# Performance work log

Hardware: AMD Instinct MI355X
Metric: run time of the kernel (lower is better)

## Reference

```python
import jax, jax.numpy as jnp
import numpy as np

NEG_INF = -1e6

def setup_inputs() -> dict:
    key = jax.random.key(0)
    ks = jax.random.split(key, 7)
    B, Q, K, D, H = 16, 64, 1024, 256, 128
    return {
        "queries": jax.random.normal(ks[0], (B, Q, D), dtype=jnp.float32),
        "keys": jax.random.normal(ks[1], (B, K, D), dtype=jnp.float32),
        "values": jax.random.normal(ks[2], (B, K, D), dtype=jnp.float32),
        "valid_lens": jax.random.randint(ks[3], (B,), 1, K + 1, dtype=jnp.int32),
        "W_q": jax.random.normal(ks[4], (D, H), dtype=jnp.float32) * (1.0 / np.sqrt(D)),
        "W_k": jax.random.normal(ks[5], (D, H), dtype=jnp.float32) * (1.0 / np.sqrt(D)),
        "w_v": jax.random.normal(ks[6], (H,), dtype=jnp.float32) * (1.0 / np.sqrt(H)),
    }

def reference(queries, keys, values, valid_lens, W_q, W_k, w_v):
    # project: [B,Q,H], [B,K,H]
    q = jnp.einsum('bqd,dh->bqh', queries, W_q)
    k = jnp.einsum('bkd,dh->bkh', keys, W_k)
    # broadcast add -> tanh -> score: [B,Q,K]
    features = jnp.tanh(q[:, :, None, :] + k[:, None, :, :])  # [B,Q,K,H]
    scores = jnp.einsum('bqkh,h->bqk', features, w_v)
    # masked softmax over key axis (valid_lens per batch)
    K_len = keys.shape[1]
    mask = jnp.arange(K_len)[None, None, :] < valid_lens[:, None, None]  # [B,1,K]
    scores = jnp.where(mask, scores, NEG_INF)
    attn = jax.nn.softmax(scores, axis=-1)
    # weighted sum of values: [B,Q,Dv]  (dropout p=0 -> identity)
    return jnp.einsum('bqk,bkd->bqd', attn, values)
```

## Files before the change

kernel.cpp:

```cpp
#include <hip/hip_runtime.h>

#define DDIM 256
#define HDIM 128
#define KLEN 1024
#define SCL 2.8853900817779268f

__global__ __launch_bounds__(256) void proj_kernel(
    const float* __restrict__ queries, const float* __restrict__ keys,
    const float* __restrict__ W_q, const float* __restrict__ W_k,
    float* __restrict__ Eq, float* __restrict__ Ek)
{
    __shared__ union {
        float a[64 * 64];
        float t[32][68];
    } sm;

    const int tid  = threadIdx.x;
    const int lane = tid & 63;
    const int wav  = tid >> 6;

    int blk = blockIdx.x;
    bool iskey; int b = 0, kc0 = 0, hb, row0;
    const float* in; const float* W;
    if (blk < 1024) {
        iskey = true;
        int xcd = blk & 7, s = blk >> 3;
        b = ((s >> 6) << 3) | xcd;
        int r6 = s & 63;
        kc0 = (r6 >> 2) << 6;
        hb  = (r6 & 3) << 5;
        row0 = b * KLEN + kc0;
        in = keys; W = W_k;
    } else {
        iskey = false;
        int qrb = blk - 1024;
        row0 = (qrb >> 2) << 6;
        hb   = (qrb & 3) << 5;
        in = queries; W = W_q;
    }

    const int hg8 = __builtin_amdgcn_readfirstlane(wav << 3);
    const float* Wu = W + hb + hg8;

    const int srow = tid >> 4;
    const int sgd  = tid & 15;
    const float* gsrc = in + (size_t)(row0 + srow) * DDIM + (sgd << 2);

    float4 pf0 = *(const float4*)(gsrc);
    float4 pf1 = *(const float4*)(gsrc + 16 * DDIM);
    float4 pf2 = *(const float4*)(gsrc + 32 * DDIM);
    float4 pf3 = *(const float4*)(gsrc + 48 * DDIM);

    float acc[8];
    #pragma unroll
    for (int c = 0; c < 8; c++) acc[c] = 0.f;

    const int w0 = (srow)      * 64 + ((sgd ^ ((srow)      & 7)) << 2);
    const int w1 = (srow + 16) * 64 + ((sgd ^ ((srow + 16) & 7)) << 2);
    const int w2 = (srow + 32) * 64 + ((sgd ^ ((srow + 32) & 7)) << 2);
    const int w3 = (srow + 48) * 64 + ((sgd ^ ((srow + 48) & 7)) << 2);

    for (int dt0 = 0; dt0 < DDIM; dt0 += 64) {
        *(float4*)(sm.a + w0) = pf0;
        *(float4*)(sm.a + w1) = pf1;
        *(float4*)(sm.a + w2) = pf2;
        *(float4*)(sm.a + w3) = pf3;
        __syncthreads();
        if (dt0 < DDIM - 64) {
            const float* g2 = gsrc + dt0 + 64;
            pf0 = *(const float4*)(g2);
            pf1 = *(const float4*)(g2 + 16 * DDIM);
            pf2 = *(const float4*)(g2 + 32 * DDIM);
            pf3 = *(const float4*)(g2 + 48 * DDIM);
        }
        const float* arow = sm.a + lane * 64;
        const int lx = lane & 7;
        #pragma unroll
        for (int d4 = 0; d4 < 64; d4 += 4) {
            float4 a = *(const float4*)(arow + ((((d4 >> 2)) ^ lx) << 2));
            const float* wr = Wu + (size_t)(dt0 + d4) * HDIM;
            #pragma unroll
            for (int c = 0; c < 8; c++) acc[c] = fmaf(a.x, wr[c],            acc[c]);
            #pragma unroll
            for (int c = 0; c < 8; c++) acc[c] = fmaf(a.y, wr[HDIM + c],     acc[c]);
            #pragma unroll
            for (int c = 0; c < 8; c++) acc[c] = fmaf(a.z, wr[2 * HDIM + c], acc[c]);
            #pragma unroll
            for (int c = 0; c < 8; c++) acc[c] = fmaf(a.w, wr[3 * HDIM + c], acc[c]);
        }
        __syncthreads();
    }

    float e[8];
    #pragma unroll
    for (int c = 0; c < 8; c++) e[c] = __builtin_amdgcn_exp2f(SCL * acc[c]);

    if (!iskey) {
        float* dst = Eq + (size_t)(row0 + lane) * HDIM + hb + hg8;
        *(float4*)(dst)     = make_float4(e[0], e[1], e[2], e[3]);
        *(float4*)(dst + 4) = make_float4(e[4], e[5], e[6], e[7]);
    } else {
        #pragma unroll
        for (int c = 0; c < 8; c++) sm.t[(wav << 3) + c][lane] = e[c];
        __syncthreads();
        float* dstb = Ek + (size_t)b * HDIM * KLEN + (size_t)hb * KLEN + kc0;
        #pragma unroll
        for (int i = 0; i < 2; i++) {
            int g = tid + (i << 8);
            int h = g >> 4, k4 = (g & 15) << 2;
            float4 o = *(const float4*)(&sm.t[h][k4]);
            *(float4*)(dstb + (size_t)h * KLEN + k4) = o;
        }
    }
}

__global__ __launch_bounds__(512) void score_kernel(
    const float* __restrict__ Eq, const float* __restrict__ Ek,
    const float* __restrict__ w_v, const int* __restrict__ valid_lens,
    float* __restrict__ p)
{
    __shared__ float4 eqw[HDIM];
    __shared__ float red0[8], red1[8];

    int tid = threadIdx.x, lane = tid & 63, wav = tid >> 6;
    int blk = blockIdx.x;
    int xcd = blk & 7, s = blk >> 3;
    int b = ((s >= 32) ? 8 : 0) + xcd;
    int qp = s & 31;
    int bq0 = b * 64 + qp * 2;
    int vlen = valid_lens[b];

    if (tid < HDIM) {
        float w2 = -2.0f * w_v[tid];
        eqw[tid] = make_float4(Eq[(size_t)bq0 * HDIM + tid],
                               Eq[(size_t)(bq0 + 1) * HDIM + tid], w2, 0.f);
    }
    __syncthreads();

    int k0 = tid << 1;
    float s00 = -1e30f, s01 = -1e30f, s10 = -1e30f, s11 = -1e30f;
    if (k0 < vlen) {
        const float* ekp = Ek + (size_t)b * HDIM * KLEN + k0;
        float a00 = 0.f, a01 = 0.f, a10 = 0.f, a11 = 0.f;
        #pragma unroll 4
        for (int h = 0; h < HDIM; h++) {
            float2 ek = *(const float2*)(ekp + (size_t)h * KLEN);
            float4 e  = eqw[h];
            a00 = fmaf(e.z, __builtin_amdgcn_rcpf(fmaf(e.x, ek.x, 1.f)), a00);
            a01 = fmaf(e.z, __builtin_amdgcn_rcpf(fmaf(e.x, ek.y, 1.f)), a01);
            a10 = fmaf(e.z, __builtin_amdgcn_rcpf(fmaf(e.y, ek.x, 1.f)), a10);
            a11 = fmaf(e.z, __builtin_amdgcn_rcpf(fmaf(e.y, ek.y, 1.f)), a11);
        }
        s00 = a00; s10 = a10;
        if (k0 + 1 < vlen) { s01 = a01; s11 = a11; }
    }

    float m0 = fmaxf(s00, s01), m1 = fmaxf(s10, s11);
    #pragma unroll
    for (int off = 32; off > 0; off >>= 1) {
        m0 = fmaxf(m0, __shfl_xor(m0, off, 64));
        m1 = fmaxf(m1, __shfl_xor(m1, off, 64));
    }
    if (lane == 0) { red0[wav] = m0; red1[wav] = m1; }
    __syncthreads();
    m0 = red0[0]; m1 = red1[0];
    #pragma unroll
    for (int i = 1; i < 8; i++) {
        m0 = fmaxf(m0, red0[i]);
        m1 = fmaxf(m1, red1[i]);
    }

    float e00 = __expf(s00 - m0), e01 = __expf(s01 - m0);
    float e10 = __expf(s10 - m1), e11 = __expf(s11 - m1);
    float t0 = e00 + e01, t1 = e10 + e11;
    #pragma unroll
    for (int off = 32; off > 0; off >>= 1) {
        t0 += __shfl_xor(t0, off, 64);
        t1 += __shfl_xor(t1, off, 64);
    }
    __syncthreads();
    if (lane == 0) { red0[wav] = t0; red1[wav] = t1; }
    __syncthreads();
    t0 = red0[0]; t1 = red1[0];
    #pragma unroll
    for (int i = 1; i < 8; i++) { t0 += red0[i]; t1 += red1[i]; }
    float inv0 = 1.0f / t0, inv1 = 1.0f / t1;

    float* p0 = p + (size_t)bq0 * KLEN + k0;
    *(float2*)(p0)        = make_float2(e00 * inv0, e01 * inv0);
    *(float2*)(p0 + KLEN) = make_float2(e10 * inv1, e11 * inv1);
}

__global__ __launch_bounds__(256) void av_kernel(
    const float* __restrict__ p, const float* __restrict__ values,
    const int* __restrict__ valid_lens, float* __restrict__ part)
{
    __shared__ union {
        float  pt[512][8];
        float4 slab[4][8][64];
    } sm;

    int blk = blockIdx.x;
    int xcd = blk & 7, s = blk >> 3;
    int b = ((s >> 4) << 3) | xcd;
    int r = s & 15, qt = r >> 1, kh = r & 1;
    int tid = threadIdx.x, lane = tid & 63, w = tid >> 6;
    int vlen = valid_lens[b];
    int bq0 = b * 64 + qt * 8;
    int kbase = kh << 9;

    #pragma unroll
    for (int i = 0; i < 4; i++) {
        int slot = tid + (i << 8);
        int q = slot >> 7, k4 = (slot & 127) << 2;
        float4 pv = *(const float4*)(p + (size_t)(bq0 + q) * KLEN + kbase + k4);
        sm.pt[k4 + 0][q] = pv.x;
        sm.pt[k4 + 1][q] = pv.y;
        sm.pt[k4 + 2][q] = pv.z;
        sm.pt[k4 + 3][q] = pv.w;
    }
    __syncthreads();

    int kw = w << 7;
    int cnt = vlen - (kbase + kw); cnt = cnt < 0 ? 0 : (cnt > 128 ? 128 : cnt);
    int cnt4 = (cnt + 3) & ~3;
    const float* vb = values + ((size_t)b * KLEN + kbase + kw) * DDIM + (lane << 2);

    float4 acc[8];
    #pragma unroll
    for (int q = 0; q < 8; q++) acc[q] = make_float4(0.f, 0.f, 0.f, 0.f);

    for (int k = 0; k < cnt4; k += 4) {
        #pragma unroll
        for (int j = 0; j < 4; j++) {
            float4 v  = *(const float4*)(vb + (size_t)(k + j) * DDIM);
            float4 p0 = *(const float4*)(&sm.pt[kw + k + j][0]);
            float4 p1 = *(const float4*)(&sm.pt[kw + k + j][4]);
            float pq[8] = {p0.x, p0.y, p0.z, p0.w, p1.x, p1.y, p1.z, p1.w};
            #pragma unroll
            for (int q = 0; q < 8; q++) {
                acc[q].x = fmaf(pq[q], v.x, acc[q].x);
                acc[q].y = fmaf(pq[q], v.y, acc[q].y);
                acc[q].z = fmaf(pq[q], v.z, acc[q].z);
                acc[q].w = fmaf(pq[q], v.w, acc[q].w);
            }
        }
    }

    __syncthreads();
    #pragma unroll
    for (int q = 0; q < 8; q++) sm.slab[w][q][lane] = acc[q];
    __syncthreads();
    #pragma unroll
    for (int e = 0; e < 2; e++) {
        int slot = (tid << 1) | e;
        int q = slot >> 6, d4 = slot & 63;
        float4 a = sm.slab[0][q][d4];
        #pragma unroll
        for (int g = 1; g < 4; g++) {
            float4 t = sm.slab[g][q][d4];
            a.x += t.x; a.y += t.y; a.z += t.z; a.w += t.w;
        }
        *(float4*)(part + ((size_t)kh * 1024 + bq0 + q) * DDIM + (d4 << 2)) = a;
    }
}

__global__ __launch_bounds__(256) void combine_kernel(
    const float* __restrict__ part, float* __restrict__ out)
{
    int i = blockIdx.x * 256 + threadIdx.x;
    const float4* p4 = (const float4*)part;
    float4 a = p4[i];
    float4 v = p4[65536 + i];
    a.x += v.x; a.y += v.y; a.z += v.z; a.w += v.w;
    ((float4*)out)[i] = a;
}

extern "C" void kernel_launch(void* const* d_in, const int* in_sizes, int n_in,
                              void* d_out, int out_size, void* d_ws, size_t ws_size,
                              hipStream_t stream) {
    const float* queries    = (const float*)d_in[0];
    const float* keys       = (const float*)d_in[1];
    const float* values     = (const float*)d_in[2];
    const int*   valid_lens = (const int*)d_in[3];
    const float* W_q        = (const float*)d_in[4];
    const float* W_k        = (const float*)d_in[5];
    const float* w_v        = (const float*)d_in[6];

    float* Eq   = (float*)d_ws;
    float* Ek   = Eq + 131072;
    float* p    = Ek + 2097152;
    float* part = Ek;

    proj_kernel<<<1088, 256, 0, stream>>>(queries, keys, W_q, W_k, Eq, Ek);
    score_kernel<<<512, 512, 0, stream>>>(Eq, Ek, w_v, valid_lens, p);
    av_kernel<<<256, 256, 0, stream>>>(p, values, valid_lens, part);
    combine_kernel<<<256, 256, 0, stream>>>(part, (float*)d_out);
}
```

Measured before the change: 147.1 us.

## Tile score kernel over 4 queries with LDS-staged Ek and defer softmax normalization

```diff
diff --git a/kernel.cpp b/kernel.cpp
--- a/kernel.cpp
+++ b/kernel.cpp
@@ -114,85 +114,108 @@
     }
 }
 
-__global__ __launch_bounds__(512) void score_kernel(
+__global__ __launch_bounds__(256) void score_kernel(
     const float* __restrict__ Eq, const float* __restrict__ Ek,
     const float* __restrict__ w_v, const int* __restrict__ valid_lens,
-    float* __restrict__ p)
+    float* __restrict__ E, float* __restrict__ T)
 {
-    __shared__ float4 eqw[HDIM];
-    __shared__ float red0[8], red1[8];
-
-    int tid = threadIdx.x, lane = tid & 63, wav = tid >> 6;
-    int blk = blockIdx.x;
-    int xcd = blk & 7, s = blk >> 3;
-    int b = ((s >= 32) ? 8 : 0) + xcd;
-    int qp = s & 31;
-    int bq0 = b * 64 + qp * 2;
+    __shared__ float ekt[8][KLEN];
+    __shared__ float eqs[4][HDIM];
+    __shared__ float w2s[HDIM];
+    __shared__ float tred[4][4];
+
+    const int tid = threadIdx.x;
+    const int lane = tid & 63, wav = tid >> 6;
+    int m = blockIdx.x;
+    int xcd = m & 7, bh = (m >> 3) & 1, qg = m >> 4;
+    int b = (bh << 3) | xcd;
+    int bq0 = b * 64 + qg * 4;
+
+    if (tid < HDIM) w2s[tid] = -2.0f * w_v[tid];
+    #pragma unroll
+    for (int i = 0; i < 2; i++) {
+        int idx = tid + (i << 8);
+        int q = idx >> 7, h = idx & 127;
+        eqs[q][h] = Eq[(size_t)(bq0 + q) * HDIM + h];
+    }
+
+    const float* ekb = Ek + (size_t)b * HDIM * KLEN;
+    const int k0 = tid << 2;
+
+    float4 pf[8];
+    #pragma unroll
+    for (int i = 0; i < 8; i++)
+        pf[i] = *(const float4*)(ekb + (size_t)i * KLEN + k0);
+
+    float4 acc4[4];
+    #pragma unroll
+    for (int j = 0; j < 4; j++) acc4[j] = make_float4(0.f, 0.f, 0.f, 0.f);
+
+    for (int c = 0; c < 16; c++) {
+        __syncthreads();
+        #pragma unroll
+        for (int i = 0; i < 8; i++)
+            *(float4*)(&ekt[i][k0]) = pf[i];
+        __syncthreads();
+        if (c < 15) {
+            const float* nx = ekb + (size_t)(c + 1) * 8 * KLEN + k0;
+            #pragma unroll
+            for (int i = 0; i < 8; i++)
+                pf[i] = *(const float4*)(nx + (size_t)i * KLEN);
+        }
+        const int c8 = c << 3;
+        float eqr[4][8], w2r[8];
+        #pragma unroll
+        for (int j = 0; j < 4; j++) {
+            *(float4*)(&eqr[j][0]) = *(const float4*)(&eqs[j][c8]);
+            *(float4*)(&eqr[j][4]) = *(const float4*)(&eqs[j][c8 + 4]);
+        }
+        *(float4*)(&w2r[0]) = *(const float4*)(&w2s[c8]);
+        *(float4*)(&w2r[4]) = *(const float4*)(&w2s[c8 + 4]);
+
+        #pragma unroll
+        for (int hh = 0; hh < 8; hh++) {
+            float4 ek = *(const float4*)(&ekt[hh][k0]);
+            float w2v = w2r[hh];
+            #pragma unroll
+            for (int j = 0; j < 4; j++) {
+                float eqv = eqr[j][hh];
+                acc4[j].x = fmaf(w2v, __builtin_amdgcn_rcpf(fmaf(eqv, ek.x, 1.f)), acc4[j].x);
+                acc4[j].y = fmaf(w2v, __builtin_amdgcn_rcpf(fmaf(eqv, ek.y, 1.f)), acc4[j].y);
+                acc4[j].z = fmaf(w2v, __builtin_amdgcn_rcpf(fmaf(eqv, ek.z, 1.f)), acc4[j].z);
+                acc4[j].w = fmaf(w2v, __builtin_amdgcn_rcpf(fmaf(eqv, ek.w, 1.f)), acc4[j].w);
+            }
+        }
+    }
+
     int vlen = valid_lens[b];
-
-    if (tid < HDIM) {
-        float w2 = -2.0f * w_v[tid];
-        eqw[tid] = make_float4(Eq[(size_t)bq0 * HDIM + tid],
-                               Eq[(size_t)(bq0 + 1) * HDIM + tid], w2, 0.f);
+    float ts[4];
+    #pragma unroll
+    for (int j = 0; j < 4; j++) {
+        float4 ev;
+        ev.x = (k0 + 0 < vlen) ? __expf(acc4[j].x) : 0.f;
+        ev.y = (k0 + 1 < vlen) ? __expf(acc4[j].y) : 0.f;
+        ev.z = (k0 + 2 < vlen) ? __expf(acc4[j].z) : 0.f;
+        ev.w = (k0 + 3 < vlen) ? __expf(acc4[j].w) : 0.f;
+        *(float4*)(E + (size_t)(bq0 + j) * KLEN + k0) = ev;
+        ts[j] = (ev.x + ev.y) + (ev.z + ev.w);
+    }
+    #pragma unroll
+    for (int j = 0; j < 4; j++) {
+        float t = ts[j];
+        #pragma unroll
+        for (int off = 32; off > 0; off >>= 1) t += __shfl_xor(t, off, 64);
+        if (lane == 0) tred[wav][j] = t;
     }
     __syncthreads();
-
-    int k0 = tid << 1;
-    float s00 = -1e30f, s01 = -1e30f, s10 = -1e30f, s11 = -1e30f;
-    if (k0 < vlen) {
-        const float* ekp = Ek + (size_t)b * HDIM * KLEN + k0;
-        float a00 = 0.f, a01 = 0.f, a10 = 0.f, a11 = 0.f;
-        #pragma unroll 4
-        for (int h = 0; h < HDIM; h++) {
-            float2 ek = *(const float2*)(ekp + (size_t)h * KLEN);
-            float4 e  = eqw[h];
-            a00 = fmaf(e.z, __builtin_amdgcn_rcpf(fmaf(e.x, ek.x, 1.f)), a00);
-            a01 = fmaf(e.z, __builtin_amdgcn_rcpf(fmaf(e.x, ek.y, 1.f)), a01);
-            a10 = fmaf(e.z, __builtin_amdgcn_rcpf(fmaf(e.y, ek.x, 1.f)), a10);
-            a11 = fmaf(e.z, __builtin_amdgcn_rcpf(fmaf(e.y, ek.y, 1.f)), a11);
-        }
-        s00 = a00; s10 = a10;
-        if (k0 + 1 < vlen) { s01 = a01; s11 = a11; }
-    }
-
-    float m0 = fmaxf(s00, s01), m1 = fmaxf(s10, s11);
-    #pragma unroll
-    for (int off = 32; off > 0; off >>= 1) {
-        m0 = fmaxf(m0, __shfl_xor(m0, off, 64));
-        m1 = fmaxf(m1, __shfl_xor(m1, off, 64));
-    }
-    if (lane == 0) { red0[wav] = m0; red1[wav] = m1; }
-    __syncthreads();
-    m0 = red0[0]; m1 = red1[0];
-    #pragma unroll
-    for (int i = 1; i < 8; i++) {
-        m0 = fmaxf(m0, red0[i]);
-        m1 = fmaxf(m1, red1[i]);
-    }
-
-    float e00 = __expf(s00 - m0), e01 = __expf(s01 - m0);
-    float e10 = __expf(s10 - m1), e11 = __expf(s11 - m1);
-    float t0 = e00 + e01, t1 = e10 + e11;
-    #pragma unroll
-    for (int off = 32; off > 0; off >>= 1) {
-        t0 += __shfl_xor(t0, off, 64);
-        t1 += __shfl_xor(t1, off, 64);
-    }
-    __syncthreads();
-    if (lane == 0) { red0[wav] = t0; red1[wav] = t1; }
-    __syncthreads();
-    t0 = red0[0]; t1 = red1[0];
-    #pragma unroll
-    for (int i = 1; i < 8; i++) { t0 += red0[i]; t1 += red1[i]; }
-    float inv0 = 1.0f / t0, inv1 = 1.0f / t1;
-
-    float* p0 = p + (size_t)bq0 * KLEN + k0;
-    *(float2*)(p0)        = make_float2(e00 * inv0, e01 * inv0);
-    *(float2*)(p0 + KLEN) = make_float2(e10 * inv1, e11 * inv1);
+    if (tid < 4) {
+        float t = tred[0][tid] + tred[1][tid] + tred[2][tid] + tred[3][tid];
+        T[bq0 + tid] = t;
+    }
 }
 
 __global__ __launch_bounds__(256) void av_kernel(
-    const float* __restrict__ p, const float* __restrict__ values,
+    const float* __restrict__ E, const float* __restrict__ values,
     const int* __restrict__ valid_lens, float* __restrict__ part)
 {
     __shared__ union {
@@ -213,7 +236,7 @@
     for (int i = 0; i < 4; i++) {
         int slot = tid + (i << 8);
         int q = slot >> 7, k4 = (slot & 127) << 2;
-        float4 pv = *(const float4*)(p + (size_t)(bq0 + q) * KLEN + kbase + k4);
+        float4 pv = *(const float4*)(E + (size_t)(bq0 + q) * KLEN + kbase + k4);
         sm.pt[k4 + 0][q] = pv.x;
         sm.pt[k4 + 1][q] = pv.y;
         sm.pt[k4 + 2][q] = pv.z;
@@ -266,13 +289,16 @@
 }
 
 __global__ __launch_bounds__(256) void combine_kernel(
-    const float* __restrict__ part, float* __restrict__ out)
+    const float* __restrict__ part, const float* __restrict__ T,
+    float* __restrict__ out)
 {
     int i = blockIdx.x * 256 + threadIdx.x;
     const float4* p4 = (const float4*)part;
     float4 a = p4[i];
     float4 v = p4[65536 + i];
-    a.x += v.x; a.y += v.y; a.z += v.z; a.w += v.w;
+    float inv = 1.0f / T[i >> 6];
+    a.x = (a.x + v.x) * inv; a.y = (a.y + v.y) * inv;
+    a.z = (a.z + v.z) * inv; a.w = (a.w + v.w) * inv;
     ((float4*)out)[i] = a;
 }
 
@@ -289,11 +315,12 @@
 
     float* Eq   = (float*)d_ws;
     float* Ek   = Eq + 131072;
-    float* p    = Ek + 2097152;
+    float* E    = Ek + 2097152;
+    float* T    = E + 1048576;
     float* part = Ek;
 
     proj_kernel<<<1088, 256, 0, stream>>>(queries, keys, W_q, W_k, Eq, Ek);
-    score_kernel<<<512, 512, 0, stream>>>(Eq, Ek, w_v, valid_lens, p);
-    av_kernel<<<256, 256, 0, stream>>>(p, values, valid_lens, part);
-    combine_kernel<<<256, 256, 0, stream>>>(part, (float*)d_out);
-}
+    score_kernel<<<256, 256, 0, stream>>>(Eq, Ek, w_v, valid_lens, E, T);
+    av_kernel<<<256, 256, 0, stream>>>(E, values, valid_lens, part);
+    combine_kernel<<<256, 256, 0, stream>>>(part, T, (float*)d_out);
+}
```

Result: slower. 195.9 us (+33.2%).
